# Kernel tuning notes

Hardware: AMD Instinct MI355X
Metric: run time of the kernel (lower is better)

Reference implementation:

```python
import jax, jax.numpy as jnp
import numpy as np

B = 4096
NP = 196  # 14*14 patches
NW = 4    # qubits


def setup_inputs() -> dict:
    key = jax.random.key(0)
    ks = jax.random.split(key, 6)
    x = jax.random.normal(ks[0], (B, 1, 28, 28), dtype=jnp.float32)
    conv_w = jax.random.normal(ks[1], (4, 1, 2, 2), dtype=jnp.float32) * 0.5
    conv_b = jax.random.normal(ks[2], (4,), dtype=jnp.float32) * 0.1
    q_theta = jax.random.uniform(ks[3], (4,), dtype=jnp.float32, minval=0.0, maxval=2.0 * np.pi)
    lin_w = jax.random.normal(ks[4], (10, 784), dtype=jnp.float32) * 0.03
    lin_b = jnp.zeros((10,), dtype=jnp.float32)
    return {"x": x, "conv_w": conv_w, "conv_b": conv_b, "q_theta": q_theta,
            "lin_w": lin_w, "lin_b": lin_b}


def _apply_1q(state, U, wire):
    # state: [N,2,2,2,2] complex, wire axis = wire+1
    s = jnp.moveaxis(state, wire + 1, -1)
    s = jnp.einsum('...a,ba->...b', s, U)
    return jnp.moveaxis(s, -1, wire + 1)


def _apply_cnot(state, ctrl, tgt):
    s = jnp.moveaxis(state, (ctrl + 1, tgt + 1), (-2, -1))  # [...,c,t]
    s = jnp.stack([s[..., 0, :], s[..., 1, ::-1]], axis=-2)
    return jnp.moveaxis(s, (-2, -1), (ctrl + 1, tgt + 1))


def _ry(t):
    c, s = jnp.cos(t), jnp.sin(t)
    return jnp.stack([jnp.stack([c, -s]), jnp.stack([s, c])]).astype(jnp.complex64)


def _rx(t):
    c, s = jnp.cos(t).astype(jnp.complex64), jnp.sin(t).astype(jnp.complex64)
    return jnp.stack([jnp.stack([c, -1j * s]), jnp.stack([-1j * s, c])])


def _rz(t):
    e = jnp.exp(-1j * t.astype(jnp.complex64))
    z = jnp.zeros((), jnp.complex64)
    return jnp.stack([jnp.stack([e, z]), jnp.stack([z, jnp.conj(e)])])


def _quantum_features(angles, q_theta):
    # angles: [N,4] encoding Ry angles; starts from |0000> per patch (encoder resets state)
    h = 0.5 * angles
    q = jnp.stack([jnp.cos(h), jnp.sin(h)], axis=-1).astype(jnp.complex64)  # [N,4,2]
    state = jnp.einsum('na,nb,nc,nd->nabcd', q[:, 0], q[:, 1], q[:, 2], q[:, 3])
    th = 0.5 * q_theta
    # fixed 8-op random layer: 4 rotations + 4 CNOTs
    state = _apply_1q(state, _ry(th[0]), 0)
    state = _apply_1q(state, _rx(th[1]), 1)
    state = _apply_1q(state, _rz(th[2]), 2)
    state = _apply_1q(state, _ry(th[3]), 3)
    state = _apply_cnot(state, 0, 1)
    state = _apply_cnot(state, 1, 2)
    state = _apply_cnot(state, 2, 3)
    state = _apply_cnot(state, 0, 3)
    probs = state.real ** 2 + state.imag ** 2  # [N,2,2,2,2]
    ez = []
    for w in range(NW):
        axes = tuple(a for a in range(1, 5) if a != w + 1)
        p = probs.sum(axis=axes)  # [N,2]
        ez.append(p[:, 0] - p[:, 1])
    return jnp.stack(ez, axis=-1)  # [N,4] <Z_w> expectations


def reference(x, conv_w, conv_b, q_theta, lin_w, lin_b):
    feats = jax.lax.conv_general_dilated(
        x, conv_w, window_strides=(2, 2), padding='VALID',
        dimension_numbers=('NCHW', 'OIHW', 'NCHW')) + conv_b[None, :, None, None]
    bsz = feats.shape[0]
    flat = feats.reshape(bsz, -1)                    # [B, 4*14*14] channel-major
    patches = flat.reshape(bsz, 14, 14, 4)           # as in torch .view
    angles = patches.reshape(bsz * NP, NW)           # patch-major over (r,c)
    qf = _quantum_features(angles, q_theta).reshape(bsz, NP * NW).astype(jnp.float32)
    logits = qf @ lin_w.T + lin_b
    return jax.nn.log_softmax(logits, axis=-1)
```

## Files before the change

### kernel.cpp

```cpp
#include <hip/hip_runtime.h>
#include <math.h>


#define NB 4096
#define NPATCH 196

__global__ __launch_bounds__(256) void hqe_kernel(
    const float* __restrict__ x,
    const float* __restrict__ conv_w,
    const float* __restrict__ conv_b,
    const float* __restrict__ q_theta,
    const float* __restrict__ lin_w,
    const float* __restrict__ lin_b,
    float* __restrict__ out)
{
    __shared__ __align__(16) float xs[784];
    __shared__ float red[4][10];
    __shared__ float logits_s[10];

    const int b = blockIdx.x;
    const int t = threadIdx.x;

    if (t < 196) {
        ((float4*)xs)[t] = ((const float4*)(x + b * 784))[t];
    }

    const float th0 = q_theta[0];
    const float ct1 = cosf(q_theta[1]);
    const float th3 = q_theta[3];

    __syncthreads();

    float partial[10];
#pragma unroll
    for (int o = 0; o < 10; ++o) partial[o] = 0.0f;

    if (t < NPATCH) {
        const int p = t;
        const int c = p / 49;
        const float4 cw = ((const float4*)conv_w)[c];
        const float cb = conv_b[c];
        const int rbase = 4 * p - 196 * c;

        float a[4];
#pragma unroll
        for (int k = 0; k < 4; ++k) {
            const int r = rbase + k;
            const int h = r / 14;
            const int w = r - 14 * h;
            const float* xp = xs + (2 * h) * 28 + 2 * w;
            a[k] = cb + xp[0] * cw.x + xp[1] * cw.y + xp[28] * cw.z + xp[29] * cw.w;
        }

        const float z0 = cosf(a[0] + th0);
        const float z1 = ct1 * cosf(a[1]);
        const float z2 = cosf(a[2]);
        const float z3 = cosf(a[3] + th3);
        const float f0 = z0;
        const float f1 = z0 * z1;
        const float f2 = f1 * z2;
        const float f3 = z1 * z2 * z3;

        const float4* w4 = (const float4*)lin_w;
#pragma unroll
        for (int o = 0; o < 10; ++o) {
            const float4 w = w4[o * 196 + p];
            partial[o] = f0 * w.x + f1 * w.y + f2 * w.z + f3 * w.w;
        }
    }

#pragma unroll
    for (int o = 0; o < 10; ++o) {
        float v = partial[o];
#pragma unroll
        for (int off = 32; off > 0; off >>= 1)
            v += __shfl_down(v, off, 64);
        partial[o] = v;
    }
    const int wave = t >> 6;
    const int lane = t & 63;
    if (lane == 0) {
#pragma unroll
        for (int o = 0; o < 10; ++o) red[wave][o] = partial[o];
    }
    __syncthreads();

    if (t < 10) {
        logits_s[t] = red[0][t] + red[1][t] + red[2][t] + red[3][t] + lin_b[t];
    }
    __syncthreads();

    if (t < 10) {
        float m = -INFINITY;
#pragma unroll
        for (int o = 0; o < 10; ++o) m = fmaxf(m, logits_s[o]);
        float s = 0.0f;
#pragma unroll
        for (int o = 0; o < 10; ++o) s += expf(logits_s[o] - m);
        out[b * 10 + t] = logits_s[t] - m - logf(s);
    }
}

extern "C" void kernel_launch(void* const* d_in, const int* in_sizes, int n_in,
                              void* d_out, int out_size, void* d_ws, size_t ws_size,
                              hipStream_t stream) {
    const float* x       = (const float*)d_in[0];
    const float* conv_w  = (const float*)d_in[1];
    const float* conv_b  = (const float*)d_in[2];
    const float* q_theta = (const float*)d_in[3];
    const float* lin_w   = (const float*)d_in[4];
    const float* lin_b   = (const float*)d_in[5];
    float* out = (float*)d_out;

    hqe_kernel<<<dim3(NB), dim3(256), 0, stream>>>(x, conv_w, conv_b, q_theta,
                                                   lin_w, lin_b, out);
}
```

Before: 82.87 us.

## Stage quantum features in LDS and compute logits per-wave over outputs

Quantum features are now written to shared memory. Each wave then computes whole logits, taking outputs o = wave, wave+4, ... and doing a full 784-length dot product with one wave reduction per logit. This replaces the old scheme where every thread computed all 10 partial sums and needed 10 cross-wave shuffle reductions plus a shared-memory combine. Fast intrinsics (__cosf, __expf, __logf) replace the precise math calls, which trades some accuracy for cheaper transcendental evaluation.

```diff
diff --git a/kernel.cpp b/kernel.cpp
--- a/kernel.cpp
+++ b/kernel.cpp
@@ -3,7 +3,6 @@
 
 
 #define NB 4096
-#define NPATCH 196
 
 __global__ __launch_bounds__(256) void hqe_kernel(
     const float* __restrict__ x,
@@ -15,89 +14,87 @@
     float* __restrict__ out)
 {
     __shared__ __align__(16) float xs[784];
-    __shared__ float red[4][10];
+    __shared__ __align__(16) float qf[784];
     __shared__ float logits_s[10];
 
     const int b = blockIdx.x;
     const int t = threadIdx.x;
+    const int wave = t >> 6;
+    const int lane = t & 63;
 
     if (t < 196) {
         ((float4*)xs)[t] = ((const float4*)(x + b * 784))[t];
+    } else if (t < 206) {
+        logits_s[t - 196] = lin_b[t - 196];
     }
 
     const float th0 = q_theta[0];
-    const float ct1 = cosf(q_theta[1]);
+    const float ct1 = __cosf(q_theta[1]);
     const float th3 = q_theta[3];
 
     __syncthreads();
 
-    float partial[10];
-#pragma unroll
-    for (int o = 0; o < 10; ++o) partial[o] = 0.0f;
-
-    if (t < NPATCH) {
-        const int p = t;
-        const int c = p / 49;
+    if (t < 196) {
+        const int c = t / 49;
+        const int rbase = 4 * t - 196 * c;
         const float4 cw = ((const float4*)conv_w)[c];
         const float cb = conv_b[c];
-        const int rbase = 4 * p - 196 * c;
-
         float a[4];
 #pragma unroll
         for (int k = 0; k < 4; ++k) {
-            const int r = rbase + k;
-            const int h = r / 14;
-            const int w = r - 14 * h;
-            const float* xp = xs + (2 * h) * 28 + 2 * w;
+            const int s = rbase + k;
+            const int h = s / 14;
+            const int w = s - 14 * h;
+            const float* xp = xs + 56 * h + 2 * w;
             a[k] = cb + xp[0] * cw.x + xp[1] * cw.y + xp[28] * cw.z + xp[29] * cw.w;
         }
-
-        const float z0 = cosf(a[0] + th0);
-        const float z1 = ct1 * cosf(a[1]);
-        const float z2 = cosf(a[2]);
-        const float z3 = cosf(a[3] + th3);
-        const float f0 = z0;
+        const float z0 = __cosf(a[0] + th0);
+        const float z1 = ct1 * __cosf(a[1]);
+        const float z2 = __cosf(a[2]);
+        const float z3 = __cosf(a[3] + th3);
         const float f1 = z0 * z1;
         const float f2 = f1 * z2;
         const float f3 = z1 * z2 * z3;
-
-        const float4* w4 = (const float4*)lin_w;
-#pragma unroll
-        for (int o = 0; o < 10; ++o) {
-            const float4 w = w4[o * 196 + p];
-            partial[o] = f0 * w.x + f1 * w.y + f2 * w.z + f3 * w.w;
-        }
+        ((float4*)qf)[t] = make_float4(z0, f1, f2, f3);
     }
 
-#pragma unroll
-    for (int o = 0; o < 10; ++o) {
-        float v = partial[o];
+    __syncthreads();
+
+    const float4* q4 = (const float4*)qf;
+    const float4 q0 = q4[lane];
+    const float4 q1 = q4[64 + lane];
+    const float4 q2 = q4[128 + lane];
+    float4 q3 = make_float4(0.f, 0.f, 0.f, 0.f);
+    if (lane < 4) q3 = q4[192 + lane];
+
+    for (int o = wave; o < 10; o += 4) {
+        const float4* wv = (const float4*)(lin_w + o * 784);
+        const float4 w0 = wv[lane];
+        const float4 w1 = wv[64 + lane];
+        const float4 w2 = wv[128 + lane];
+        float s = q0.x * w0.x + q0.y * w0.y + q0.z * w0.z + q0.w * w0.w;
+        s += q1.x * w1.x + q1.y * w1.y + q1.z * w1.z + q1.w * w1.w;
+        s += q2.x * w2.x + q2.y * w2.y + q2.z * w2.z + q2.w * w2.w;
+        if (lane < 4) {
+            const float4 w3 = wv[192 + lane];
+            s += q3.x * w3.x + q3.y * w3.y + q3.z * w3.z + q3.w * w3.w;
+        }
 #pragma unroll
         for (int off = 32; off > 0; off >>= 1)
-            v += __shfl_down(v, off, 64);
-        partial[o] = v;
+            s += __shfl_down(s, off, 64);
+        if (lane == 0) logits_s[o] += s;
     }
-    const int wave = t >> 6;
-    const int lane = t & 63;
-    if (lane == 0) {
-#pragma unroll
-        for (int o = 0; o < 10; ++o) red[wave][o] = partial[o];
-    }
-    __syncthreads();
 
-    if (t < 10) {
-        logits_s[t] = red[0][t] + red[1][t] + red[2][t] + red[3][t] + lin_b[t];
-    }
     __syncthreads();
 
     if (t < 10) {
         float m = -INFINITY;
 #pragma unroll
-        for (int o = 0; o < 10; ++o) m = fmaxf(m, logits_s[o]);
-        float s = 0.0f;
+        for (int j = 0; j < 10; ++j) m = fmaxf(m, logits_s[j]);
+        float sum = 0.0f;
 #pragma unroll
-        for (int o = 0; o < 10; ++o) s += expf(logits_s[o] - m);
-        out[b * 10 + t] = logits_s[t] - m - logf(s);
+        for (int j = 0; j < 10; ++j) sum += __expf(logits_s[j] - m);
+        out[b * 10 + t] = logits_s[t] - m - __logf(sum);
     }
 }
 
```

Result: faster. 78.41 us (-5.4%).
